# Kernel tuning notes

Hardware: AMD Instinct MI355X
Metric: run time of the kernel (lower is better)

The kernel has to match this reference:

```python
import jax, jax.numpy as jnp
import numpy as np

D_MODEL = 1024
N_HEADS = 16
D_K = D_MODEL // N_HEADS
B, S = 4, 2048


def setup_inputs() -> dict:
    key = jax.random.key(0)
    ks = jax.random.split(key, 5)
    scale = 1.0 / np.sqrt(D_MODEL)  # ~xavier scale for square matrices
    return {
        "Q": jax.random.normal(ks[0], (B, S, D_MODEL), dtype=jnp.float32),
        "length": jax.random.randint(ks[1], (B,), 1, S, dtype=jnp.int32),
        "Wq": jax.random.normal(ks[2], (D_MODEL, D_MODEL), dtype=jnp.float32) * scale,
        "bq": jnp.zeros((D_MODEL,), dtype=jnp.float32),
        "Wk": jax.random.normal(ks[3], (D_MODEL, D_MODEL), dtype=jnp.float32) * scale,
        "bk": jnp.zeros((D_MODEL,), dtype=jnp.float32),
        "Wv": jax.random.normal(ks[4], (D_MODEL, D_MODEL), dtype=jnp.float32) * scale,
        "bv": jnp.zeros((D_MODEL,), dtype=jnp.float32),
    }


def reference(Q, length, Wq, bq, Wk, bk, Wv, bv):
    b, s, d = Q.shape
    q_a = Q @ Wq + bq                                   # [b, s, d]
    # split heads: [b, h, s, d_k]
    q_s = q_a.reshape(b, s, N_HEADS, D_K).transpose(0, 2, 1, 3)
    k_s = (Q @ Wk + bk).reshape(b, s, N_HEADS, D_K).transpose(0, 2, 1, 3)
    v_s = (Q @ Wv + bv).reshape(b, s, N_HEADS, D_K).transpose(0, 2, 1, 3)

    # unnormalized exp attention with multiplicative key mask (faithful to source)
    scores = jnp.einsum("bhqd,bhkd->bhqk", q_s, k_s) / np.sqrt(D_K)
    scores = jnp.exp(scores)
    key_mask = (jnp.arange(s)[None, :] < length[:, None]).astype(scores.dtype)  # [b, k]
    scores = scores * key_mask[:, None, None, :]        # broadcast over heads, queries
    attn = scores / (jnp.sum(scores, axis=-1, keepdims=True) + 1e-8)
    context = jnp.einsum("bhqk,bhkd->bhqd", attn, v_s)
    context = context.transpose(0, 2, 1, 3).reshape(b, s, d)
    return context, q_a
```

## Files before the change

kernel.cpp:

```cpp
#include <hip/hip_runtime.h>

#define D_MODEL 1024
#define N_HEADS 16
#define D_KH    64
#define BATCH   4
#define SEQ     2048
#define M_TOTAL (BATCH*SEQ)

typedef __attribute__((ext_vector_type(8))) short short8;
typedef __attribute__((ext_vector_type(4))) float f32x4;
typedef __attribute__((ext_vector_type(4))) unsigned short u16x4;
typedef __attribute__((ext_vector_type(2))) unsigned int u32x2;

__device__ __forceinline__ unsigned short f2bf(float f) {
  union { float f; unsigned u; } v; v.f = f;
  unsigned r = v.u + 0x7FFFu + ((v.u >> 16) & 1u);
  return (unsigned short)(r >> 16);
}
__device__ __forceinline__ unsigned fbits(float f) {
  union { float f; unsigned u; } v; v.f = f; return v.u;
}

__global__ __launch_bounds__(256) void cvt_q(const float* __restrict__ Q,
                                             unsigned short* __restrict__ Qbf) {
  size_t i = (size_t)blockIdx.x * 256 + threadIdx.x;
  float4 v = ((const float4*)Q)[i];
  u16x4 o;
  o[0] = f2bf(v.x); o[1] = f2bf(v.y); o[2] = f2bf(v.z); o[3] = f2bf(v.w);
  ((u16x4*)Qbf)[i] = o;
}

__global__ __launch_bounds__(256) void cvt_wt(const float* __restrict__ Wq,
                                              const float* __restrict__ Wk,
                                              const float* __restrict__ Wv,
                                              unsigned short* __restrict__ WT) {
  const int z = blockIdx.z;
  const float* W = (z == 0) ? Wq : (z == 1) ? Wk : Wv;
  __shared__ float tile[32][33];
  const int k0 = blockIdx.y * 32, n0 = blockIdx.x * 32;
  const int tx = threadIdx.x & 31, ty = threadIdx.x >> 5;
  for (int i = 0; i < 4; ++i)
    tile[ty + i * 8][tx] = W[(size_t)(k0 + ty + i * 8) * D_MODEL + n0 + tx];
  __syncthreads();
  unsigned short* out = WT + (size_t)z * D_MODEL * D_MODEL;
  for (int i = 0; i < 4; ++i)
    out[(size_t)(n0 + ty + i * 8) * D_MODEL + k0 + tx] = f2bf(tile[tx][ty + i * 8]);
}

#define BM 128
#define BN 128
#define BK 32

__global__ __launch_bounds__(256, 2) void gemm_qkv(
    const unsigned short* __restrict__ Qbf,
    const unsigned short* __restrict__ WT,
    const float* __restrict__ bq_p, const float* __restrict__ bk_p,
    const float* __restrict__ bv_p,
    float* __restrict__ out_qa,
    unsigned short* __restrict__ kbf,
    unsigned short* __restrict__ vt) {
  const int z  = blockIdx.z;
  const int n0 = blockIdx.x * BN;
  const int m0 = blockIdx.y * BM;
  const int K  = D_MODEL;

  __shared__ unsigned short smA[BM * BK];
  __shared__ unsigned short smB[BN * BK];

  const int t    = threadIdx.x;
  const int lane = t & 63;
  const int w    = t >> 6;
  const int quad = lane >> 4;
  const int l16  = lane & 15;
  const int wr   = w >> 1, wc = w & 1;

  const unsigned short* Wz = WT + (size_t)z * D_MODEL * D_MODEL;

  f32x4 acc[4][4];
  for (int i = 0; i < 4; ++i)
    for (int j = 0; j < 4; ++j) acc[i][j] = (f32x4){0.f, 0.f, 0.f, 0.f};

  for (int k0 = 0; k0 < K; k0 += BK) {
    __syncthreads();
    for (int it = 0; it < 2; ++it) {
      int c   = t + it * 256;
      int row = c >> 2, col = (c & 3) * 8;
      const unsigned short* ga = Qbf + (size_t)(m0 + row) * K + k0 + col;
      const unsigned short* gb = Wz  + (size_t)(n0 + row) * K + k0 + col;
      __builtin_amdgcn_global_load_lds(
          (const __attribute__((address_space(1))) void*)ga,
          (__attribute__((address_space(3))) void*)&smA[c * 8], 16, 0, 0);
      __builtin_amdgcn_global_load_lds(
          (const __attribute__((address_space(1))) void*)gb,
          (__attribute__((address_space(3))) void*)&smB[c * 8], 16, 0, 0);
    }
    __syncthreads();

    short8 afr[4], bfr[4];
    for (int mi = 0; mi < 4; ++mi)
      afr[mi] = *(const short8*)&smA[(wr * 64 + mi * 16 + l16) * BK + quad * 8];
    for (int ni = 0; ni < 4; ++ni)
      bfr[ni] = *(const short8*)&smB[(wc * 64 + ni * 16 + l16) * BK + quad * 8];
    for (int mi = 0; mi < 4; ++mi)
      for (int ni = 0; ni < 4; ++ni)
        acc[mi][ni] = __builtin_amdgcn_mfma_f32_16x16x32_bf16(
            afr[mi], bfr[ni], acc[mi][ni], 0, 0, 0);
  }

  const float* bias = (z == 0) ? bq_p : (z == 1) ? bk_p : bv_p;
  if (z == 2) {
    for (int ni = 0; ni < 4; ++ni) {
      int n = n0 + wc * 64 + ni * 16 + l16;
      float bval = bias[n];
      int h = n >> 6, d = n & 63;
      for (int mi = 0; mi < 4; ++mi) {
        int m = m0 + wr * 64 + mi * 16 + quad * 4;
        int b = m >> 11, s = m & 2047;
        u16x4 o;
        for (int j = 0; j < 4; ++j) o[j] = f2bf(acc[mi][ni][j] + bval);
        *(u16x4*)&vt[(size_t)((b * 16 + h) * 64 + d) * SEQ + s] = o;
      }
    }
  } else {
    for (int ni = 0; ni < 4; ++ni) {
      int n = n0 + wc * 64 + ni * 16 + l16;
      float bval = bias[n];
      for (int mi = 0; mi < 4; ++mi) {
        int mbase = m0 + wr * 64 + mi * 16 + quad * 4;
        for (int j = 0; j < 4; ++j) {
          float v = acc[mi][ni][j] + bval;
          size_t idx = (size_t)(mbase + j) * D_MODEL + n;
          if (z == 0) out_qa[idx] = v;
          else        kbf[idx] = f2bf(v);
        }
      }
    }
  }
}

#define PST 72
#define QBLK 128

__global__ __launch_bounds__(256, 4) void attn(
    const float* __restrict__ qa,
    const unsigned short* __restrict__ kbf,
    const unsigned short* __restrict__ vt,
    const int* __restrict__ length,
    float* __restrict__ ctx) {
  const int flat = blockIdx.y * 16 + blockIdx.x;
  const int low = flat & 3;
  const int mid = (flat >> 2) & 15;
  const int hi  = flat >> 6;
  const int b  = (low + mid + (mid >> 2) + hi + (hi >> 2)) & 3;
  const int h  = mid;
  const int qt = hi;
  const int bh = b * 16 + h;
  const int len = length[b];

  const int t    = threadIdx.x;
  const int lane = t & 63;
  const int w    = t >> 6;
  const int quad = lane >> 4;
  const int l16  = lane & 15;
  const int r8   = t >> 3;
  const int c8   = (t & 7) * 8;

  __shared__ unsigned short sQ[QBLK * PST];
  __shared__ unsigned short sK[64 * PST];
  __shared__ unsigned short sVT[64 * PST];
  unsigned short* const sP = sQ;

  const float SCL = 0.125f * 1.44269504f;

  for (int half = 0; half < 4; ++half) {
    int r = r8 + half * 32;
    const float* src = qa + (size_t)(b * SEQ + qt * QBLK + r) * D_MODEL + h * D_KH + c8;
    float4 v0 = *(const float4*)src;
    float4 v1 = *(const float4*)(src + 4);
    short8 o;
    o[0] = (short)f2bf(v0.x * SCL); o[1] = (short)f2bf(v0.y * SCL);
    o[2] = (short)f2bf(v0.z * SCL); o[3] = (short)f2bf(v0.w * SCL);
    o[4] = (short)f2bf(v1.x * SCL); o[5] = (short)f2bf(v1.y * SCL);
    o[6] = (short)f2bf(v1.z * SCL); o[7] = (short)f2bf(v1.w * SCL);
    *(short8*)&sQ[r * PST + c8] = o;
  }
  __syncthreads();

  short8 qf00 = *(const short8*)&sQ[(w * 16 + l16) * PST + quad * 8];
  short8 qf01 = *(const short8*)&sQ[(w * 16 + l16) * PST + 32 + quad * 8];
  short8 qf10 = *(const short8*)&sQ[(64 + w * 16 + l16) * PST + quad * 8];
  short8 qf11 = *(const short8*)&sQ[(64 + w * 16 + l16) * PST + 32 + quad * 8];

  f32x4 acc0[4], acc1[4];
  for (int i = 0; i < 4; ++i) {
    acc0[i] = (f32x4){0.f, 0.f, 0.f, 0.f};
    acc1[i] = (f32x4){0.f, 0.f, 0.f, 0.f};
  }
  float den0 = 0.f, den1 = 0.f;

  const unsigned short* kbase_p = kbf + (size_t)b * SEQ * D_MODEL + h * D_KH;
  const unsigned short* vbase_p = vt + (size_t)bh * 64 * SEQ;

  const int nkt = (len + 63) >> 6;

  short8 rk[2], rv[2];
  for (int half = 0; half < 2; ++half) {
    int r = r8 + half * 32;
    rk[half] = *(const short8*)(kbase_p + (size_t)r * D_MODEL + c8);
    rv[half] = *(const short8*)(vbase_p + (size_t)r * SEQ + c8);
  }

  for (int kt = 0; kt < nkt; ++kt) {
    __syncthreads();
    for (int half = 0; half < 2; ++half) {
      int r = r8 + half * 32;
      *(short8*)&sK[r * PST + c8]  = rk[half];
      *(short8*)&sVT[r * PST + c8] = rv[half];
    }
    __syncthreads();

    if (kt + 1 < nkt) {
      for (int half = 0; half < 2; ++half) {
        int r = r8 + half * 32;
        rk[half] = *(const short8*)(kbase_p + (size_t)((kt + 1) * 64 + r) * D_MODEL + c8);
        rv[half] = *(const short8*)(vbase_p + (size_t)r * SEQ + (kt + 1) * 64 + c8);
      }
    }

    const bool full = ((kt + 1) << 6) <= len;

    for (int n = 0; n < 4; ++n) {
      short8 kf0 = *(const short8*)&sK[(n * 16 + l16) * PST + quad * 8];
      short8 kf1 = *(const short8*)&sK[(n * 16 + l16) * PST + 32 + quad * 8];
      f32x4 s0 = (f32x4){0.f, 0.f, 0.f, 0.f};
      s0 = __builtin_amdgcn_mfma_f32_16x16x32_bf16(kf0, qf00, s0, 0, 0, 0);
      s0 = __builtin_amdgcn_mfma_f32_16x16x32_bf16(kf1, qf01, s0, 0, 0, 0);
      f32x4 s1 = (f32x4){0.f, 0.f, 0.f, 0.f};
      s1 = __builtin_amdgcn_mfma_f32_16x16x32_bf16(kf0, qf10, s1, 0, 0, 0);
      s1 = __builtin_amdgcn_mfma_f32_16x16x32_bf16(kf1, qf11, s1, 0, 0, 0);

      float e0, e1, e2, e3, f0, f1, f2, f3;
      if (full) {
        e0 = exp2f(s0[0]); e1 = exp2f(s0[1]); e2 = exp2f(s0[2]); e3 = exp2f(s0[3]);
        f0 = exp2f(s1[0]); f1 = exp2f(s1[1]); f2 = exp2f(s1[2]); f3 = exp2f(s1[3]);
      } else {
        int kb = kt * 64 + n * 16 + quad * 4;
        e0 = (kb + 0 < len) ? exp2f(s0[0]) : 0.f;
        e1 = (kb + 1 < len) ? exp2f(s0[1]) : 0.f;
        e2 = (kb + 2 < len) ? exp2f(s0[2]) : 0.f;
        e3 = (kb + 3 < len) ? exp2f(s0[3]) : 0.f;
        f0 = (kb + 0 < len) ? exp2f(s1[0]) : 0.f;
        f1 = (kb + 1 < len) ? exp2f(s1[1]) : 0.f;
        f2 = (kb + 2 < len) ? exp2f(s1[2]) : 0.f;
        f3 = (kb + 3 < len) ? exp2f(s1[3]) : 0.f;
      }
      den0 += (e0 + e1) + (e2 + e3);
      den1 += (f0 + f1) + (f2 + f3);
      u32x2 pk;
      pk[0] = __builtin_amdgcn_perm(fbits(e1), fbits(e0), 0x07060302);
      pk[1] = __builtin_amdgcn_perm(fbits(e3), fbits(e2), 0x07060302);
      *(u32x2*)&sP[(w * 16 + l16) * PST + n * 16 + quad * 4] = pk;
      u32x2 pk1;
      pk1[0] = __builtin_amdgcn_perm(fbits(f1), fbits(f0), 0x07060302);
      pk1[1] = __builtin_amdgcn_perm(fbits(f3), fbits(f2), 0x07060302);
      *(u32x2*)&sP[(64 + w * 16 + l16) * PST + n * 16 + quad * 4] = pk1;
    }

    short8 pf00 = *(const short8*)&sP[(w * 16 + l16) * PST + quad * 8];
    short8 pf01 = *(const short8*)&sP[(w * 16 + l16) * PST + 32 + quad * 8];
    short8 pf10 = *(const short8*)&sP[(64 + w * 16 + l16) * PST + quad * 8];
    short8 pf11 = *(const short8*)&sP[(64 + w * 16 + l16) * PST + 32 + quad * 8];
    for (int n2 = 0; n2 < 4; ++n2) {
      short8 vf0 = *(const short8*)&sVT[(n2 * 16 + l16) * PST + quad * 8];
      short8 vf1 = *(const short8*)&sVT[(n2 * 16 + l16) * PST + 32 + quad * 8];
      acc0[n2] = __builtin_amdgcn_mfma_f32_16x16x32_bf16(vf0, pf00, acc0[n2], 0, 0, 0);
      acc0[n2] = __builtin_amdgcn_mfma_f32_16x16x32_bf16(vf1, pf01, acc0[n2], 0, 0, 0);
      acc1[n2] = __builtin_amdgcn_mfma_f32_16x16x32_bf16(vf0, pf10, acc1[n2], 0, 0, 0);
      acc1[n2] = __builtin_amdgcn_mfma_f32_16x16x32_bf16(vf1, pf11, acc1[n2], 0, 0, 0);
    }
  }

  den0 += __shfl_xor(den0, 16, 64);
  den0 += __shfl_xor(den0, 32, 64);
  den1 += __shfl_xor(den1, 16, 64);
  den1 += __shfl_xor(den1, 32, 64);
  float inv0 = 1.f / (den0 + 1e-8f);
  float inv1 = 1.f / (den1 + 1e-8f);

  {
    int q0 = qt * QBLK + w * 16 + l16;
    float* dst0 = ctx + (size_t)(b * SEQ + q0) * D_MODEL + h * D_KH;
    float* dst1 = dst0 + (size_t)64 * D_MODEL;
    for (int n2 = 0; n2 < 4; ++n2) {
      f32x4 o0 = acc0[n2];
      f32x4 o1 = acc1[n2];
      *(float4*)(dst0 + n2 * 16 + quad * 4) =
          make_float4(o0[0] * inv0, o0[1] * inv0, o0[2] * inv0, o0[3] * inv0);
      *(float4*)(dst1 + n2 * 16 + quad * 4) =
          make_float4(o1[0] * inv1, o1[1] * inv1, o1[2] * inv1, o1[3] * inv1);
    }
  }
}

extern "C" void kernel_launch(void* const* d_in, const int* in_sizes, int n_in,
                              void* d_out, int out_size, void* d_ws, size_t ws_size,
                              hipStream_t stream) {
  const float* Q      = (const float*)d_in[0];
  const int*   length = (const int*)d_in[1];
  const float* Wq     = (const float*)d_in[2];
  const float* bq     = (const float*)d_in[3];
  const float* Wk     = (const float*)d_in[4];
  const float* bk     = (const float*)d_in[5];
  const float* Wv     = (const float*)d_in[6];
  const float* bv     = (const float*)d_in[7];

  float* out_ctx = (float*)d_out;
  float* out_qa  = out_ctx + (size_t)M_TOTAL * D_MODEL;

  char* ws = (char*)d_ws;
  unsigned short* Qbf = (unsigned short*)ws;
  unsigned short* WT  = (unsigned short*)(ws + (size_t)16 * 1024 * 1024);
  unsigned short* Kbf = (unsigned short*)(ws + (size_t)22 * 1024 * 1024);
  unsigned short* Vt  = (unsigned short*)(ws + (size_t)38 * 1024 * 1024);

  hipLaunchKernelGGL(cvt_q, dim3((M_TOTAL * D_MODEL) / (256 * 4)), dim3(256), 0, stream,
                     Q, Qbf);
  hipLaunchKernelGGL(cvt_wt, dim3(32, 32, 3), dim3(256), 0, stream, Wq, Wk, Wv, WT);
  hipLaunchKernelGGL(gemm_qkv, dim3(D_MODEL / BN, M_TOTAL / BM, 3), dim3(256), 0, stream,
                     Qbf, WT, bq, bk, bv, out_qa, Kbf, Vt);
  hipLaunchKernelGGL(attn, dim3(SEQ / QBLK, BATCH * N_HEADS), dim3(256), 0, stream,
                     out_qa, Kbf, Vt, length, out_ctx);
}
```

Measured before the change: 255.8 us.

## Double-buffer QKV GEMM with swizzled LDS, BK=64, and XCD-aware block mapping

Rewrites the QKV projection GEMM main loop to use double-buffered LDS tiles with BK=64. Global-to-LDS loads for tile k+2 are issued while tile k is being computed, and explicit vmcnt waits plus barriers replace the per-step sync pairs. LDS addresses are XOR-swizzled to avoid bank conflicts. The grid is flattened to 1D with a remap that spreads blocks across the eight XCDs and treats the three weight matrices as one N=3072 GEMM. LDS use doubles to 64KB per block, which may limit occupancy to the two blocks per CU requested by launch bounds.

```diff
diff --git a/kernel.cpp b/kernel.cpp
--- a/kernel.cpp
+++ b/kernel.cpp
@@ -47,9 +47,10 @@
     out[(size_t)(n0 + ty + i * 8) * D_MODEL + k0 + tx] = f2bf(tile[tx][ty + i * 8]);
 }
 
-#define BM 128
-#define BN 128
-#define BK 32
+#define GQ_BM 128
+#define GQ_BN 128
+#define GQ_BK 64
+#define GQ_NT (D_MODEL / GQ_BK)
 
 __global__ __launch_bounds__(256, 2) void gemm_qkv(
     const unsigned short* __restrict__ Qbf,
@@ -59,13 +60,17 @@
     float* __restrict__ out_qa,
     unsigned short* __restrict__ kbf,
     unsigned short* __restrict__ vt) {
-  const int z  = blockIdx.z;
-  const int n0 = blockIdx.x * BN;
-  const int m0 = blockIdx.y * BM;
-  const int K  = D_MODEL;
-
-  __shared__ unsigned short smA[BM * BK];
-  __shared__ unsigned short smB[BN * BK];
+  const int f   = blockIdx.x;
+  const int swz = (f & 7) * 192 + (f >> 3);
+  const int mm  = swz / 24;
+  const int nn  = swz % 24;
+  const int m0  = mm * GQ_BM;
+  const int n0g = nn * GQ_BN;
+  const int z   = n0g >> 10;
+  const int n0  = n0g & 1023;
+
+  __shared__ unsigned short smA[2][GQ_BM * GQ_BK];
+  __shared__ unsigned short smB[2][GQ_BN * GQ_BK];
 
   const int t    = threadIdx.x;
   const int lane = t & 63;
@@ -74,37 +79,76 @@
   const int l16  = lane & 15;
   const int wr   = w >> 1, wc = w & 1;
 
-  const unsigned short* Wz = WT + (size_t)z * D_MODEL * D_MODEL;
-
   f32x4 acc[4][4];
   for (int i = 0; i < 4; ++i)
     for (int j = 0; j < 4; ++j) acc[i][j] = (f32x4){0.f, 0.f, 0.f, 0.f};
 
-  for (int k0 = 0; k0 < K; k0 += BK) {
-    __syncthreads();
-    for (int it = 0; it < 2; ++it) {
-      int c   = t + it * 256;
-      int row = c >> 2, col = (c & 3) * 8;
-      const unsigned short* ga = Qbf + (size_t)(m0 + row) * K + k0 + col;
-      const unsigned short* gb = Wz  + (size_t)(n0 + row) * K + k0 + col;
+  auto stage = [&](int p, int kt) {
+    #pragma unroll
+    for (int r = 0; r < 4; ++r) {
+      int o   = (r * 256 + t) * 8;
+      int row = o >> 6;
+      int col = (o & 63) ^ ((row & 7) << 3);
+      const unsigned short* ga = Qbf + (size_t)(m0 + row)  * D_MODEL + kt * 64 + col;
+      const unsigned short* gb = WT  + (size_t)(n0g + row) * D_MODEL + kt * 64 + col;
       __builtin_amdgcn_global_load_lds(
           (const __attribute__((address_space(1))) void*)ga,
-          (__attribute__((address_space(3))) void*)&smA[c * 8], 16, 0, 0);
+          (__attribute__((address_space(3))) void*)&smA[p][o], 16, 0, 0);
       __builtin_amdgcn_global_load_lds(
           (const __attribute__((address_space(1))) void*)gb,
-          (__attribute__((address_space(3))) void*)&smB[c * 8], 16, 0, 0);
-    }
-    __syncthreads();
-
-    short8 afr[4], bfr[4];
+          (__attribute__((address_space(3))) void*)&smB[p][o], 16, 0, 0);
+    }
+  };
+
+  stage(0, 0);
+  stage(1, 1);
+  asm volatile("s_waitcnt vmcnt(8)" ::: "memory");
+  __builtin_amdgcn_s_barrier();
+  asm volatile("" ::: "memory");
+
+  for (int kt = 0; kt < GQ_NT; ++kt) {
+    const int p = kt & 1;
+
+    short8 af[4][2], bf[4][2];
+    #pragma unroll
+    for (int mi = 0; mi < 4; ++mi) {
+      int row = wr * 64 + mi * 16 + l16;
+      #pragma unroll
+      for (int kk = 0; kk < 2; ++kk)
+        af[mi][kk] = *(const short8*)
+            &smA[p][(row * 64 + kk * 32 + quad * 8) ^ ((row & 7) << 3)];
+    }
+    #pragma unroll
+    for (int ni = 0; ni < 4; ++ni) {
+      int row = wc * 64 + ni * 16 + l16;
+      #pragma unroll
+      for (int kk = 0; kk < 2; ++kk)
+        bf[ni][kk] = *(const short8*)
+            &smB[p][(row * 64 + kk * 32 + quad * 8) ^ ((row & 7) << 3)];
+    }
+
+    __builtin_amdgcn_s_setprio(1);
+    #pragma unroll
     for (int mi = 0; mi < 4; ++mi)
-      afr[mi] = *(const short8*)&smA[(wr * 64 + mi * 16 + l16) * BK + quad * 8];
-    for (int ni = 0; ni < 4; ++ni)
-      bfr[ni] = *(const short8*)&smB[(wc * 64 + ni * 16 + l16) * BK + quad * 8];
-    for (int mi = 0; mi < 4; ++mi)
-      for (int ni = 0; ni < 4; ++ni)
+      #pragma unroll
+      for (int ni = 0; ni < 4; ++ni) {
         acc[mi][ni] = __builtin_amdgcn_mfma_f32_16x16x32_bf16(
-            afr[mi], bfr[ni], acc[mi][ni], 0, 0, 0);
+            af[mi][0], bf[ni][0], acc[mi][ni], 0, 0, 0);
+        acc[mi][ni] = __builtin_amdgcn_mfma_f32_16x16x32_bf16(
+            af[mi][1], bf[ni][1], acc[mi][ni], 0, 0, 0);
+      }
+    __builtin_amdgcn_s_setprio(0);
+
+    __builtin_amdgcn_s_barrier();
+    asm volatile("" ::: "memory");
+    if (kt + 2 < GQ_NT) {
+      stage(p, kt + 2);
+      asm volatile("s_waitcnt vmcnt(8)" ::: "memory");
+    } else {
+      asm volatile("s_waitcnt vmcnt(0)" ::: "memory");
+    }
+    __builtin_amdgcn_s_barrier();
+    asm volatile("" ::: "memory");
   }
 
   const float* bias = (z == 0) ? bq_p : (z == 1) ? bk_p : bv_p;
@@ -326,7 +370,7 @@
   hipLaunchKernelGGL(cvt_q, dim3((M_TOTAL * D_MODEL) / (256 * 4)), dim3(256), 0, stream,
                      Q, Qbf);
   hipLaunchKernelGGL(cvt_wt, dim3(32, 32, 3), dim3(256), 0, stream, Wq, Wk, Wv, WT);
-  hipLaunchKernelGGL(gemm_qkv, dim3(D_MODEL / BN, M_TOTAL / BM, 3), dim3(256), 0, stream,
+  hipLaunchKernelGGL(gemm_qkv, dim3(64 * 24), dim3(256), 0, stream,
                      Qbf, WT, bq, bk, bv, out_qa, Kbf, Vt);
   hipLaunchKernelGGL(attn, dim3(SEQ / QBLK, BATCH * N_HEADS), dim3(256), 0, stream,
                      out_qa, Kbf, Vt, length, out_ctx);
```

New measurement: 243.5 us. 4.8% less time.
